# Performance work log

Hardware: AMD Instinct MI355X
Metric: run time of the kernel (lower is better)

The kernel has to match this reference:

```python
import jax, jax.numpy as jnp
import numpy as np

B = 1 << 20  # batch rows
H = 2        # LSTM input_size = hidden_size = 2
K = 11       # number of parallel LSTMs
C = 34       # classifier input size (11*2 + 12 others)
C15 = 51     # int(34 * 1.5)
P = 5        # toPredict_size


def setup_inputs() -> dict:
    key = jax.random.key(0)
    ks = jax.random.split(key, 12)
    s = 0.1
    inp = {
        "input_data": jax.random.normal(ks[0], (B, C), dtype=jnp.float32),
        # Per-LSTM input->gates weights, PyTorch gate order (i, f, g, o): [K, 4H, H]
        "W_ih": jax.random.normal(ks[1], (K, 4 * H, H), dtype=jnp.float32) * s,
        "b_ih": jax.random.normal(ks[2], (K, 4 * H), dtype=jnp.float32) * s,
        # h0 = 0 so W_hh contributes nothing; only its bias b_hh matters.
        "b_hh": jax.random.normal(ks[3], (K, 4 * H), dtype=jnp.float32) * s,
        "W1": jax.random.normal(ks[4], (C15, C), dtype=jnp.float32) * s,
        "b1": jax.random.normal(ks[5], (C15,), dtype=jnp.float32) * s,
        "W2": jax.random.normal(ks[6], (C15, C15), dtype=jnp.float32) * s,
        "b2": jax.random.normal(ks[7], (C15,), dtype=jnp.float32) * s,
        "W3": jax.random.normal(ks[8], (C, C15), dtype=jnp.float32) * s,
        "b3": jax.random.normal(ks[9], (C,), dtype=jnp.float32) * s,
        "W4": jax.random.normal(ks[10], (P, C), dtype=jnp.float32) * s,
        "b4": jax.random.normal(ks[11], (P,), dtype=jnp.float32) * s,
    }
    return inp


def _lstm_heads(x, W_ih, b_ih, b_hh):
    # x: [B, K, H]; single-step LSTM from zero state for each of K heads.
    gates = jnp.einsum("bkh,kgh->bkg", x, W_ih) + b_ih + b_hh  # [B, K, 4H]
    i, f, g, o = jnp.split(gates, 4, axis=-1)  # each [B, K, H]
    c = jax.nn.sigmoid(i) * jnp.tanh(g)        # f*c0 = 0 since c0 = 0
    h = jax.nn.sigmoid(o) * jnp.tanh(c)
    return h  # [B, K, H]


def reference(input_data, W_ih, b_ih, b_hh, W1, b1, W2, b2, W3, b3, W4, b4):
    bsz = input_data.shape[0]
    x_seqs = input_data[:, : K * H].reshape(bsz, K, H)
    others = input_data[:, K * H :]  # [B, 12]
    h = _lstm_heads(x_seqs, W_ih, b_ih, b_hh).reshape(bsz, K * H)
    cated = jnp.concatenate([h, others], axis=-1)  # [B, 34]
    z = jax.nn.relu(cated @ W1.T + b1)
    z = jax.nn.relu(z @ W2.T + b2)
    z = jax.nn.relu(z @ W3.T + b3)
    out = jax.nn.sigmoid(z @ W4.T + b4)  # [B, 5]
    return out
```

## Files before the change

### kernel.cpp

```cpp
#include <hip/hip_runtime.h>


#define BLK  256
#define WPB  4
#define KSEQ 11

typedef _Float16 h2   __attribute__((ext_vector_type(2)));
typedef _Float16 h8   __attribute__((ext_vector_type(8)));
typedef float    f4   __attribute__((ext_vector_type(4)));
typedef unsigned u16v __attribute__((ext_vector_type(16)));

#define N_FRAG_U32 6144
#define N_BIAS     768
#define N_LSTM     288

__device__ __align__(16) float    g_lstm[N_LSTM];
__device__ __align__(16) unsigned g_frag[N_FRAG_U32];
__device__ __align__(16) unsigned g_bias[N_BIAS];

__device__ __forceinline__ h2 pk(float a, float b) {
    auto r = __builtin_amdgcn_cvt_pkrtz(a, b);
    union { decltype(r) f; h2 h; } c; c.f = r; return c.h;
}
__device__ __forceinline__ unsigned as_u32(h2 h) {
    union { h2 h; unsigned u; } c; c.h = h; return c.u;
}
__device__ __forceinline__ float uf(unsigned u) {
    union { unsigned u; float f; } c; c.u = u; return c.f;
}
__device__ __forceinline__ unsigned pkrelu(float a, float b) {
    h2 p = pk(a, b);
    h2 z = {(_Float16)0.0f, (_Float16)0.0f};
    h2 r = __builtin_elementwise_max(p, z);
    return as_u32(r);
}
__device__ __forceinline__ float fast_exp(float x) {
#if __has_builtin(__builtin_amdgcn_exp2f)
    return __builtin_amdgcn_exp2f(x * 1.44269504088896340736f);
#else
    return __expf(x);
#endif
}
__device__ __forceinline__ float fast_rcp(float x) {
#if __has_builtin(__builtin_amdgcn_rcpf)
    return __builtin_amdgcn_rcpf(x);
#else
    return 1.0f / x;
#endif
}
__device__ __forceinline__ float sig1(float x)  { return fast_rcp(1.0f + fast_exp(-x)); }

__device__ __forceinline__ float sigtanh(float a, float b) {
    float ea = fast_exp(-a);
    float eb = fast_exp(2.0f * b);
    return (eb - 1.0f) * fast_rcp((1.0f + ea) * (eb + 1.0f));
}

__device__ __forceinline__ void sload3(const unsigned* p, u16v& c0, u16v& c1, u16v& c2) {
    asm volatile("s_load_dwordx16 %0, %3, 0x0\n\t"
                 "s_load_dwordx16 %1, %3, 0x40\n\t"
                 "s_load_dwordx16 %2, %3, 0x80\n\t"
                 "s_waitcnt lgkmcnt(0)"
                 : "=&s"(c0), "=&s"(c1), "=&s"(c2) : "s"(p));
}
__device__ __forceinline__ unsigned pick48(const u16v& c0, const u16v& c1, const u16v& c2, int j) {
    return j < 16 ? c0[j] : (j < 32 ? c1[j - 16] : c2[j - 32]);
}

__device__ __forceinline__ void lstm_one(const u16v& c0, const u16v& c1, const u16v& c2, int base,
                                         float2 x, h2& outp)
{
    float w0  = uf(pick48(c0, c1, c2, base + 0)),  w1  = uf(pick48(c0, c1, c2, base + 1));
    float w2  = uf(pick48(c0, c1, c2, base + 2)),  w3  = uf(pick48(c0, c1, c2, base + 3));
    float w8  = uf(pick48(c0, c1, c2, base + 8)),  w9  = uf(pick48(c0, c1, c2, base + 9));
    float w10 = uf(pick48(c0, c1, c2, base + 10)), w11 = uf(pick48(c0, c1, c2, base + 11));
    float w12 = uf(pick48(c0, c1, c2, base + 12)), w13 = uf(pick48(c0, c1, c2, base + 13));
    float w14 = uf(pick48(c0, c1, c2, base + 14)), w15 = uf(pick48(c0, c1, c2, base + 15));
    float B0  = uf(pick48(c0, c1, c2, base + 16)), B1v = uf(pick48(c0, c1, c2, base + 17));
    float B4  = uf(pick48(c0, c1, c2, base + 20)), B5  = uf(pick48(c0, c1, c2, base + 21));
    float B6  = uf(pick48(c0, c1, c2, base + 22)), B7  = uf(pick48(c0, c1, c2, base + 23));

    float x0 = x.x, x1 = x.y;
    float gi0 = B0  + x0 * w0  + x1 * w1;
    float gi1 = B1v + x0 * w2  + x1 * w3;
    float gg0 = B4  + x0 * w8  + x1 * w9;
    float gg1 = B5  + x0 * w10 + x1 * w11;
    float go0 = B6  + x0 * w12 + x1 * w13;
    float go1 = B7  + x0 * w14 + x1 * w15;
    float cc0 = sigtanh(gi0, gg0);
    float cc1 = sigtanh(gi1, gg1);
    float h0  = sigtanh(go0, cc0);
    float h1  = sigtanh(go1, cc1);
    outp = pk(h0, h1);
}

__global__ void prep_weights(const float* __restrict__ W_ih, const float* __restrict__ b_ih,
                             const float* __restrict__ b_hh,
                             const float* __restrict__ W1, const float* __restrict__ b1,
                             const float* __restrict__ W2, const float* __restrict__ b2,
                             const float* __restrict__ W3, const float* __restrict__ b3,
                             const float* __restrict__ W4, const float* __restrict__ b4)
{
    const int gid = blockIdx.x * blockDim.x + threadIdx.x;
    const int gs  = gridDim.x * blockDim.x;

    for (int i = gid; i < N_FRAG_U32; i += gs) {
        int t = i >> 8, rlo = i & 255;
        int lane = rlo >> 2, j = rlo & 3;
        const float* W; int N, K, ld, ks, nt;
        if (t < 8)       { W = W1; N = 51; K = 34; ld = 34; ks = t >> 2;     nt = t & 3; }
        else if (t < 16) { W = W2; N = 51; K = 51; ld = 51; ks = (t-8) >> 2; nt = (t-8) & 3; }
        else if (t < 22) { W = W3; N = 34; K = 51; ld = 51; ks = (t-16) / 3; nt = (t-16) % 3; }
        else             { W = W4; N = 5;  K = 34; ld = 34; ks = t - 22;     nt = 0; }
        int n = nt * 16 + (lane & 15);
        int p = ks * 16 + (lane >> 4) * 4 + j;
        int k_lo, k_hi;
        if (t < 8) { k_lo = 2 * p;                              k_hi = k_lo + 1;  }
        else       { k_lo = (p & 1) ? 32 + (p >> 1) : (p >> 1); k_hi = k_lo + 16; }
        float a = (n < N && k_lo < K) ? W[n * ld + k_lo] : 0.f;
        float b = (n < N && k_hi < K) ? W[n * ld + k_hi] : 0.f;
        g_frag[i] = as_u32(pk(a, b));
    }
    for (int i = gid; i < N_BIAS; i += gs) {
        int bt = i >> 6, lane = i & 63;
        const float* bv; int N, nt;
        if (bt < 4)       { bv = b1; N = 51; nt = bt; }
        else if (bt < 8)  { bv = b2; N = 51; nt = bt - 4; }
        else if (bt < 11) { bv = b3; N = 34; nt = bt - 8; }
        else              { bv = b4; N = 5;  nt = 0; }
        int col = nt * 16 + (lane & 15);
        g_bias[i] = __float_as_uint(col < N ? bv[col] : 0.f);
    }
    for (int i = gid; i < N_LSTM; i += gs) {
        int k = i / 24, cc = i - k * 24;
        float v = 0.f;
        if (k < KSEQ) v = (cc < 16) ? W_ih[k * 16 + cc]
                                    : b_ih[k * 8 + (cc - 16)] + b_hh[k * 8 + (cc - 16)];
        g_lstm[i] = v;
    }
}

__device__ __forceinline__ h8 load_frag(int tile, int l) {
    union { uint4 u; h8 h; } u;
    u.u = *(const uint4*)&g_frag[tile * 256 + l * 4];
    return u.h;
}

__device__ __forceinline__ void read_afrags(h8 (&a)[4][2], const unsigned* my, int l)
{
    const int c = l & 15, g = l >> 4;
    const int mrd = (c & 7) << 2;
    #pragma unroll
    for (int mt = 0; mt < 4; ++mt)
      #pragma unroll
      for (int ks = 0; ks < 2; ++ks) {
        int idx = (mt * 16 + c) * 32 + ((ks * 16 + g * 4) ^ mrd);
        union { uint4 u; h8 h; } u;
        u.u = *(const uint4*)&my[idx];
        a[mt][ks] = u.h;
      }
}

template<int NT, int TBASE, int BBASE>
__device__ __forceinline__ void layer_mfma(const h8 (&a)[4][2], f4 (&acc)[4][4],
                                           const float (&bs)[12], int l)
{
    #pragma unroll
    for (int mt = 0; mt < 4; ++mt)
      #pragma unroll
      for (int nt = 0; nt < NT; ++nt) {
        float b = bs[BBASE + nt];
        acc[mt][nt] = f4{b, b, b, b};
      }
    #pragma unroll
    for (int ks = 0; ks < 2; ++ks)
      #pragma unroll
      for (int nt = 0; nt < NT; ++nt) {
        h8 bf = load_frag(TBASE + ks * NT + nt, l);
        #pragma unroll
        for (int mt = 0; mt < 4; ++mt)
          acc[mt][nt] = __builtin_amdgcn_mfma_f32_16x16x32_f16(a[mt][ks], bf, acc[mt][nt], 0, 0, 0);
      }
}

template<int NT>
__device__ __forceinline__ void spill_act(const f4 (&acc)[4][4], unsigned* my, int l)
{
    const int g = l >> 4, c = l & 15;
    #pragma unroll
    for (int mt = 0; mt < 4; ++mt)
      #pragma unroll
      for (int r = 0; r < 4; ++r) {
        const int row  = mt * 16 + g * 4 + r;
        const int rowm = (row & 7) << 2;
        uint2 q;
        q.x = pkrelu(acc[mt][0][r], acc[mt][1][r]);
        float d3 = (NT >= 4) ? acc[mt][3][r] : 0.f;
        q.y = pkrelu(acc[mt][2][r], d3);
        *(uint2*)&my[row * 32 + ((2 * c) ^ rowm)] = q;
      }
}

__global__ __launch_bounds__(BLK, 3)
void fused_rnn_mlp(const float* __restrict__ in, float* __restrict__ out, int nrows)
{
    __shared__ unsigned act[WPB * 2048];
    const int tid = threadIdx.x;
    const int w = tid >> 6, l = tid & 63;
    unsigned* my = &act[w * 2048];
    const long long rb = (long long)blockIdx.x * BLK;
    if (rb + BLK > nrows) return;
    const long long rw = rb + w * 64;

    float bs[12];
    #pragma unroll
    for (int i = 0; i < 12; ++i) bs[i] = uf(g_bias[i * 64 + l]);

    float2 x[17];
    {
        const float2* rp = (const float2*)(in + (rw + l) * 34);
        #pragma unroll
        for (int i = 0; i < 17; ++i) x[i] = rp[i];
    }

    unsigned cp[32];
    #pragma unroll
    for (int kp = 0; kp < 6; ++kp) {
        u16v c0, c1, c2;
        sload3((const unsigned*)&g_lstm[kp * 48], c0, c1, c2);
        h2 h;
        lstm_one(c0, c1, c2, 0, x[2 * kp], h);
        cp[2 * kp] = as_u32(h);
        if (kp < 5) {
            lstm_one(c0, c1, c2, 24, x[2 * kp + 1], h);
            cp[2 * kp + 1] = as_u32(h);
        }
    }
    #pragma unroll
    for (int t = 0; t < 6; ++t) cp[11 + t] = as_u32(pk(x[11 + t].x, x[11 + t].y));
    #pragma unroll
    for (int t = 17; t < 32; ++t) cp[t] = 0u;

    {
        const int m = (l & 7) << 2;
        #pragma unroll
        for (int ch = 0; ch < 8; ++ch) {
            uint4 q = make_uint4(cp[4*ch], cp[4*ch+1], cp[4*ch+2], cp[4*ch+3]);
            *(uint4*)&my[l * 32 + ((4 * ch) ^ m)] = q;
        }
    }

    h8 a[4][2];
    f4 acc[4][4];

    read_afrags(a, my, l);
    layer_mfma<4, 0, 0>(a, acc, bs, l);
    spill_act<4>(acc, my, l);

    read_afrags(a, my, l);
    layer_mfma<4, 8, 4>(a, acc, bs, l);
    spill_act<4>(acc, my, l);

    read_afrags(a, my, l);
    layer_mfma<3, 16, 8>(a, acc, bs, l);
    spill_act<3>(acc, my, l);

    read_afrags(a, my, l);
    layer_mfma<1, 22, 11>(a, acc, bs, l);

    {
        const int c = l & 15, g = l >> 4;
        float* po = (float*)my;
        if (c < 5) {
            #pragma unroll
            for (int mt = 0; mt < 4; ++mt)
              #pragma unroll
              for (int r = 0; r < 4; ++r)
                po[(mt * 16 + g * 4 + r) * 9 + c] = acc[mt][0][r];
        }
    }
    __syncthreads();

    const long long ob = rb * 5;
    const float* pact = (const float*)act;
    #pragma unroll
    for (int it = 0; it < 5; ++it) {
        int F   = it * BLK + tid;
        int row = (F * 52429) >> 18;
        int cc  = F - row * 5;
        out[ob + F] = sig1(pact[(row >> 6) * 2048 + (row & 63) * 9 + cc]);
    }
}

extern "C" void kernel_launch(void* const* d_in, const int* in_sizes, int n_in,
                              void* d_out, int out_size, void* d_ws, size_t ws_size,
                              hipStream_t stream)
{
    const float* input = (const float*)d_in[0];
    const float* W_ih  = (const float*)d_in[1];
    const float* b_ih  = (const float*)d_in[2];
    const float* b_hh  = (const float*)d_in[3];
    const float* W1    = (const float*)d_in[4];
    const float* b1    = (const float*)d_in[5];
    const float* W2    = (const float*)d_in[6];
    const float* b2    = (const float*)d_in[7];
    const float* W3    = (const float*)d_in[8];
    const float* b3    = (const float*)d_in[9];
    const float* W4    = (const float*)d_in[10];
    const float* b4    = (const float*)d_in[11];
    float* out = (float*)d_out;

    int nrows = in_sizes[0] / 34;
    int grid  = nrows / BLK;

    hipLaunchKernelGGL(prep_weights, dim3(8), dim3(256), 0, stream,
                       W_ih, b_ih, b_hh, W1, b1, W2, b2, W3, b3, W4, b4);
    hipLaunchKernelGGL(fused_rnn_mlp, dim3(grid), dim3(BLK), 0, stream,
                       input, out, nrows);
}
```

Before: 60.13 us.

## Swap MFMA operand roles so layer outputs feed next layer in registers

Computes each layer as W·act^T instead of act·W^T, making weights the A operand and activations the B operand. With a permuted K ordering in the weight fragments, the accumulator layout of one layer matches the B-fragment layout of the next, so activations are repacked in registers instead of round-tripping through LDS between layers. Biases become per-lane float4 fragments loaded from global memory and used directly as the initial accumulator. This removes three LDS write/read passes per layer transition, at the cost of a more intricate weight permutation that must be exactly right.

```diff
diff --git a/kernel.cpp b/kernel.cpp
--- a/kernel.cpp
+++ b/kernel.cpp
@@ -11,12 +11,12 @@
 typedef unsigned u16v __attribute__((ext_vector_type(16)));
 
 #define N_FRAG_U32 6144
-#define N_BIAS     768
+#define N_BIAS     3072
 #define N_LSTM     288
 
 __device__ __align__(16) float    g_lstm[N_LSTM];
 __device__ __align__(16) unsigned g_frag[N_FRAG_U32];
-__device__ __align__(16) unsigned g_bias[N_BIAS];
+__device__ __align__(16) float    g_bias[N_BIAS];
 
 __device__ __forceinline__ h2 pk(float a, float b) {
     auto r = __builtin_amdgcn_cvt_pkrtz(a, b);
@@ -112,24 +112,31 @@
         else if (t < 16) { W = W2; N = 51; K = 51; ld = 51; ks = (t-8) >> 2; nt = (t-8) & 3; }
         else if (t < 22) { W = W3; N = 34; K = 51; ld = 51; ks = (t-16) / 3; nt = (t-16) % 3; }
         else             { W = W4; N = 5;  K = 34; ld = 34; ks = t - 22;     nt = 0; }
-        int n = nt * 16 + (lane & 15);
-        int p = ks * 16 + (lane >> 4) * 4 + j;
+        int m = nt * 16 + (lane & 15);
         int k_lo, k_hi;
-        if (t < 8) { k_lo = 2 * p;                              k_hi = k_lo + 1;  }
-        else       { k_lo = (p & 1) ? 32 + (p >> 1) : (p >> 1); k_hi = k_lo + 16; }
-        float a = (n < N && k_lo < K) ? W[n * ld + k_lo] : 0.f;
-        float b = (n < N && k_hi < K) ? W[n * ld + k_hi] : 0.f;
+        if (t < 8) {
+            int p = ks * 16 + (lane >> 4) * 4 + j;
+            k_lo = 2 * p; k_hi = k_lo + 1;
+        } else {
+            int q = ks * 32 + (lane >> 4) * 8 + 2 * j;
+            k_lo = (2 * (q >> 5) + ((q & 7) >> 2)) * 16 + ((q >> 3) & 3) * 4 + (q & 3);
+            int q1 = q + 1;
+            k_hi = (2 * (q1 >> 5) + ((q1 & 7) >> 2)) * 16 + ((q1 >> 3) & 3) * 4 + (q1 & 3);
+        }
+        float a = (m < N && k_lo < K) ? W[m * ld + k_lo] : 0.f;
+        float b = (m < N && k_hi < K) ? W[m * ld + k_hi] : 0.f;
         g_frag[i] = as_u32(pk(a, b));
     }
     for (int i = gid; i < N_BIAS; i += gs) {
-        int bt = i >> 6, lane = i & 63;
-        const float* bv; int N, nt;
-        if (bt < 4)       { bv = b1; N = 51; nt = bt; }
-        else if (bt < 8)  { bv = b2; N = 51; nt = bt - 4; }
-        else if (bt < 11) { bv = b3; N = 34; nt = bt - 8; }
-        else              { bv = b4; N = 5;  nt = 0; }
-        int col = nt * 16 + (lane & 15);
-        g_bias[i] = __float_as_uint(col < N ? bv[col] : 0.f);
+        int bt = i >> 8, rem = i & 255;
+        int lane = rem >> 2, r = rem & 3;
+        const float* bv; int N, ot;
+        if (bt < 4)       { bv = b1; N = 51; ot = bt; }
+        else if (bt < 8)  { bv = b2; N = 51; ot = bt - 4; }
+        else if (bt < 11) { bv = b3; N = 34; ot = bt - 8; }
+        else              { bv = b4; N = 5;  ot = 0; }
+        int n = ot * 16 + (lane >> 4) * 4 + r;
+        g_bias[i] = (n < N) ? bv[n] : 0.f;
     }
     for (int i = gid; i < N_LSTM; i += gs) {
         int k = i / 24, cc = i - k * 24;
@@ -146,59 +153,70 @@
     return u.h;
 }
 
-__device__ __forceinline__ void read_afrags(h8 (&a)[4][2], const unsigned* my, int l)
+__device__ __forceinline__ void read_bfrags(h8 (&bf)[4][2], const unsigned* my, int l)
 {
     const int c = l & 15, g = l >> 4;
     const int mrd = (c & 7) << 2;
     #pragma unroll
-    for (int mt = 0; mt < 4; ++mt)
+    for (int st = 0; st < 4; ++st)
       #pragma unroll
       for (int ks = 0; ks < 2; ++ks) {
-        int idx = (mt * 16 + c) * 32 + ((ks * 16 + g * 4) ^ mrd);
+        int idx = (st * 16 + c) * 32 + ((ks * 16 + g * 4) ^ mrd);
         union { uint4 u; h8 h; } u;
         u.u = *(const uint4*)&my[idx];
-        a[mt][ks] = u.h;
+        bf[st][ks] = u.h;
       }
 }
 
 template<int NT, int TBASE, int BBASE>
-__device__ __forceinline__ void layer_mfma(const h8 (&a)[4][2], f4 (&acc)[4][4],
-                                           const float (&bs)[12], int l)
-{
-    #pragma unroll
-    for (int mt = 0; mt < 4; ++mt)
+__device__ __forceinline__ void layer_swapped(const h8 (&bf)[4][2], f4 (&acc)[4][4], int l)
+{
+    #pragma unroll
+    for (int ot = 0; ot < NT; ++ot) {
+        f4 bias4 = *(const f4*)&g_bias[(BBASE + ot) * 256 + l * 4];
+        h8 af = load_frag(TBASE + ot, l);
+        #pragma unroll
+        for (int st = 0; st < 4; ++st)
+          acc[ot][st] = __builtin_amdgcn_mfma_f32_16x16x32_f16(af, bf[st][0], bias4, 0, 0, 0);
+    }
+    #pragma unroll
+    for (int ot = 0; ot < NT; ++ot) {
+        h8 af = load_frag(TBASE + NT + ot, l);
+        #pragma unroll
+        for (int st = 0; st < 4; ++st)
+          acc[ot][st] = __builtin_amdgcn_mfma_f32_16x16x32_f16(af, bf[st][1], acc[ot][st], 0, 0, 0);
+    }
+}
+
+template<int NT>
+__device__ __forceinline__ void pack_bfrags(const f4 (&acc)[4][4], h8 (&bf)[4][2])
+{
+    #pragma unroll
+    for (int st = 0; st < 4; ++st)
       #pragma unroll
-      for (int nt = 0; nt < NT; ++nt) {
-        float b = bs[BBASE + nt];
-        acc[mt][nt] = f4{b, b, b, b};
+      for (int ks = 0; ks < 2; ++ks) {
+        const int o0 = 2 * ks, o1 = 2 * ks + 1;
+        union { unsigned u[4]; h8 h; } cvt;
+        cvt.u[0] = pkrelu(acc[o0][st][0], acc[o0][st][1]);
+        cvt.u[1] = pkrelu(acc[o0][st][2], acc[o0][st][3]);
+        if (o1 < NT) {
+            cvt.u[2] = pkrelu(acc[o1][st][0], acc[o1][st][1]);
+            cvt.u[3] = pkrelu(acc[o1][st][2], acc[o1][st][3]);
+        } else {
+            cvt.u[2] = 0u; cvt.u[3] = 0u;
+        }
+        bf[st][ks] = cvt.h;
       }
-    #pragma unroll
-    for (int ks = 0; ks < 2; ++ks)
-      #pragma unroll
-      for (int nt = 0; nt < NT; ++nt) {
-        h8 bf = load_frag(TBASE + ks * NT + nt, l);
-        #pragma unroll
-        for (int mt = 0; mt < 4; ++mt)
-          acc[mt][nt] = __builtin_amdgcn_mfma_f32_16x16x32_f16(a[mt][ks], bf, acc[mt][nt], 0, 0, 0);
-      }
-}
-
-template<int NT>
-__device__ __forceinline__ void spill_act(const f4 (&acc)[4][4], unsigned* my, int l)
-{
-    const int g = l >> 4, c = l & 15;
-    #pragma unroll
-    for (int mt = 0; mt < 4; ++mt)
-      #pragma unroll
-      for (int r = 0; r < 4; ++r) {
-        const int row  = mt * 16 + g * 4 + r;
-        const int rowm = (row & 7) << 2;
-        uint2 q;
-        q.x = pkrelu(acc[mt][0][r], acc[mt][1][r]);
-        float d3 = (NT >= 4) ? acc[mt][3][r] : 0.f;
-        q.y = pkrelu(acc[mt][2][r], d3);
-        *(uint2*)&my[row * 32 + ((2 * c) ^ rowm)] = q;
-      }
+}
+
+__device__ __forceinline__ void stage0(const unsigned (&cp)[32], unsigned* my, int l)
+{
+    const int m = (l & 7) << 2;
+    #pragma unroll
+    for (int ch = 0; ch < 8; ++ch) {
+        uint4 q = make_uint4(cp[4*ch], cp[4*ch+1], cp[4*ch+2], cp[4*ch+3]);
+        *(uint4*)&my[l * 32 + ((4 * ch) ^ m)] = q;
+    }
 }
 
 __global__ __launch_bounds__(BLK, 3)
@@ -211,10 +229,6 @@
     const long long rb = (long long)blockIdx.x * BLK;
     if (rb + BLK > nrows) return;
     const long long rw = rb + w * 64;
-
-    float bs[12];
-    #pragma unroll
-    for (int i = 0; i < 12; ++i) bs[i] = uf(g_bias[i * 64 + l]);
 
     float2 x[17];
     {
@@ -241,42 +255,31 @@
     #pragma unroll
     for (int t = 17; t < 32; ++t) cp[t] = 0u;
 
-    {
-        const int m = (l & 7) << 2;
-        #pragma unroll
-        for (int ch = 0; ch < 8; ++ch) {
-            uint4 q = make_uint4(cp[4*ch], cp[4*ch+1], cp[4*ch+2], cp[4*ch+3]);
-            *(uint4*)&my[l * 32 + ((4 * ch) ^ m)] = q;
-        }
-    }
-
-    h8 a[4][2];
+    stage0(cp, my, l);
+
+    h8 bf[4][2];
     f4 acc[4][4];
 
-    read_afrags(a, my, l);
-    layer_mfma<4, 0, 0>(a, acc, bs, l);
-    spill_act<4>(acc, my, l);
-
-    read_afrags(a, my, l);
-    layer_mfma<4, 8, 4>(a, acc, bs, l);
-    spill_act<4>(acc, my, l);
-
-    read_afrags(a, my, l);
-    layer_mfma<3, 16, 8>(a, acc, bs, l);
-    spill_act<3>(acc, my, l);
-
-    read_afrags(a, my, l);
-    layer_mfma<1, 22, 11>(a, acc, bs, l);
+    read_bfrags(bf, my, l);
+    layer_swapped<4, 0, 0>(bf, acc, l);
+    pack_bfrags<4>(acc, bf);
+    layer_swapped<4, 8, 4>(bf, acc, l);
+    pack_bfrags<4>(acc, bf);
+    layer_swapped<3, 16, 8>(bf, acc, l);
+    pack_bfrags<3>(acc, bf);
+    layer_swapped<1, 22, 11>(bf, acc, l);
 
     {
         const int c = l & 15, g = l >> 4;
         float* po = (float*)my;
-        if (c < 5) {
+        #pragma unroll
+        for (int st = 0; st < 4; ++st) {
+            const int sample = st * 16 + c;
             #pragma unroll
-            for (int mt = 0; mt < 4; ++mt)
-              #pragma unroll
-              for (int r = 0; r < 4; ++r)
-                po[(mt * 16 + g * 4 + r) * 9 + c] = acc[mt][0][r];
+            for (int r = 0; r < 4; ++r) {
+                int n = g * 4 + r;
+                if (n < 5) po[sample * 9 + n] = acc[0][st][r];
+            }
         }
     }
     __syncthreads();
```

Result: faster. 53.10 us (-11.7%).
